# Optimization experiments

Measured on AMD Instinct MI355X. Metric: run time of the kernel, lower is better.

## Reference

```python
import jax, jax.numpy as jnp
import numpy as np

GROUPS = 32
EPS = 1e-5


def setup_inputs() -> dict:
    key = jax.random.key(0)
    ks = jax.random.split(key, 4)
    B, C, H, W = 4, 256, 64, 64
    x = jax.random.normal(ks[0], (B, C, H, W), dtype=jnp.float32)
    gn_w = jnp.ones((C,), jnp.float32)
    gn_b = jnp.zeros((C,), jnp.float32)
    qkv_w = jax.random.normal(ks[1], (3 * C, C), dtype=jnp.float32) * (C ** -0.5)
    qkv_b = jnp.zeros((3 * C,), jnp.float32)
    proj_w = jax.random.normal(ks[2], (C, C), dtype=jnp.float32) * (C ** -0.5)
    proj_b = jnp.zeros((C,), jnp.float32)
    return {"x": x, "gn_w": gn_w, "gn_b": gn_b, "qkv_w": qkv_w,
            "qkv_b": qkv_b, "proj_w": proj_w, "proj_b": proj_b}


def _group_norm(x, w, b):
    B, C, H, W = x.shape
    xr = x.reshape(B, GROUPS, -1)                      # [B, G, (C/G)*H*W]
    mean = xr.mean(axis=-1, keepdims=True)
    var = xr.var(axis=-1, keepdims=True)               # biased, like torch
    h = ((xr - mean) * jax.lax.rsqrt(var + EPS)).reshape(B, C, H, W)
    return h * w[None, :, None, None] + b[None, :, None, None]


def reference(x, gn_w, gn_b, qkv_w, qkv_b, proj_w, proj_b):
    B, C, H, W = x.shape
    h = _group_norm(x, gn_w, gn_b)
    # 1x1 conv == channel GEMM
    qkv = jnp.einsum('oc,bchw->bohw', qkv_w, h) + qkv_b[None, :, None, None]
    qkv = qkv.reshape(B, 3, C, H * W)
    q, k, v = qkv[:, 0], qkv[:, 1], qkv[:, 2]          # [B, C, N]
    scale = C ** (-0.5)
    attn = jax.nn.softmax(jnp.einsum('bci,bcj->bij', q, k) * scale, axis=-1)
    out = jnp.einsum('bij,bcj->bci', attn, v).reshape(B, C, H, W)
    out = jnp.einsum('oc,bchw->bohw', proj_w, out) + proj_b[None, :, None, None]
    return x + out
```

## Files before the change

kernel.cpp:

```cpp
#include <hip/hip_runtime.h>
#include <hip/hip_bf16.h>
#include <math.h>

typedef __bf16 bf16;
typedef __bf16 bf16x8 __attribute__((ext_vector_type(8)));
typedef __bf16 bf16x4 __attribute__((ext_vector_type(4)));
typedef float f32x4 __attribute__((ext_vector_type(4)));
typedef float f32x16 __attribute__((ext_vector_type(16)));

#define MFMA16(a, b, c) __builtin_amdgcn_mfma_f32_16x16x32_bf16(a, b, c, 0, 0, 0)
#define MFMA32(a, b, c) __builtin_amdgcn_mfma_f32_32x32x16_bf16(a, b, c, 0, 0, 0)

#define SCALEK 0.09016844005555896f

typedef const __attribute__((address_space(1))) void* gas_t;
typedef __attribute__((address_space(3))) void* las_t;

__global__ __launch_bounds__(256) void gn_kernel(
    const float* __restrict__ x, const float* __restrict__ gw,
    const float* __restrict__ gb, bf16* __restrict__ h) {
  const int bg = blockIdx.x;
  const int b = bg >> 5, g = bg & 31;
  const size_t base = (size_t)(b * 256 + g * 8) * 4096;
  const float* xp = x + base;
  bf16* hp = h + base;
  const int tid = threadIdx.x;

  float s = 0.f, ss = 0.f;
  for (int i = tid * 4; i < 32768; i += 1024) {
    float4 v = *(const float4*)(xp + i);
    s += v.x + v.y + v.z + v.w;
    ss += v.x * v.x + v.y * v.y + v.z * v.z + v.w * v.w;
  }
#pragma unroll
  for (int off = 32; off; off >>= 1) {
    s += __shfl_down(s, off);
    ss += __shfl_down(ss, off);
  }
  __shared__ float red[8];
  if ((tid & 63) == 0) {
    red[(tid >> 6) * 2] = s;
    red[(tid >> 6) * 2 + 1] = ss;
  }
  __syncthreads();
  s = red[0] + red[2] + red[4] + red[6];
  ss = red[1] + red[3] + red[5] + red[7];
  const float mean = s * (1.f / 32768.f);
  const float var = ss * (1.f / 32768.f) - mean * mean;
  const float rstd = rsqrtf(var + 1e-5f);

  for (int i = tid * 4; i < 32768; i += 1024) {
    float4 v = *(const float4*)(xp + i);
    int c = g * 8 + (i >> 12);
    float a = gw[c] * rstd;
    float b2 = gb[c] - mean * a;
    bf16x4 o;
    o[0] = (bf16)(v.x * a + b2);
    o[1] = (bf16)(v.y * a + b2);
    o[2] = (bf16)(v.z * a + b2);
    o[3] = (bf16)(v.w * a + b2);
    *(bf16x4*)(hp + i) = o;
  }
}

__global__ __launch_bounds__(256) void qkv_gemm(
    const bf16* __restrict__ h, const float* __restrict__ w,
    const float* __restrict__ bias, bf16* __restrict__ qt,
    bf16* __restrict__ kt, bf16* __restrict__ vcm) {
  const int b = blockIdx.z;
  const int o0 = blockIdx.y * 64;
  const int p0 = blockIdx.x * 64;
  __shared__ bf16 Alds[64][56];
  __shared__ bf16 Blds[64][56];
  const int tid = threadIdx.x;
  const int lane = tid & 63, wid = tid >> 6;
  const int lr = lane & 15, lg = lane >> 4;
  const int wm = wid >> 1, wn = wid & 1;
  const bf16* hb = h + (size_t)b * 256 * 4096;

  f32x4 acc[2][2] = {};

  for (int k0 = 0; k0 < 256; k0 += 32) {
    {
      int row = tid >> 2, c8 = (tid & 3) * 8;
      const float* src = w + (size_t)(o0 + row) * 256 + k0 + c8;
      float4 v0 = *(const float4*)src;
      float4 v1 = *(const float4*)(src + 4);
      bf16x8 bv;
      bv[0] = (bf16)v0.x; bv[1] = (bf16)v0.y; bv[2] = (bf16)v0.z; bv[3] = (bf16)v0.w;
      bv[4] = (bf16)v1.x; bv[5] = (bf16)v1.y; bv[6] = (bf16)v1.z; bv[7] = (bf16)v1.w;
      *(bf16x8*)&Alds[row][c8] = bv;
    }
    {
      int cc = tid >> 3, p8 = (tid & 7) * 8;
      bf16x8 v = *(const bf16x8*)(hb + (size_t)(k0 + cc) * 4096 + p0 + p8);
#pragma unroll
      for (int e = 0; e < 8; ++e) Blds[p8 + e][cc] = v[e];
    }
    __syncthreads();
    bf16x8 af[2], bfr[2];
#pragma unroll
    for (int mi = 0; mi < 2; ++mi)
      af[mi] = *(const bf16x8*)&Alds[wm * 32 + mi * 16 + lr][lg * 8];
#pragma unroll
    for (int ni = 0; ni < 2; ++ni)
      bfr[ni] = *(const bf16x8*)&Blds[wn * 32 + ni * 16 + lr][lg * 8];
#pragma unroll
    for (int mi = 0; mi < 2; ++mi)
#pragma unroll
      for (int ni = 0; ni < 2; ++ni)
        acc[mi][ni] = MFMA16(af[mi], bfr[ni], acc[mi][ni]);
    __syncthreads();
  }

#pragma unroll
  for (int mi = 0; mi < 2; ++mi) {
#pragma unroll
    for (int ni = 0; ni < 2; ++ni) {
#pragma unroll
      for (int r = 0; r < 4; ++r) {
        int o = o0 + wm * 32 + mi * 16 + lg * 4 + r;
        int p = p0 + wn * 32 + ni * 16 + lr;
        float val = acc[mi][ni][r] + bias[o];
        if (o < 256) {
          qt[((size_t)b * 4096 + p) * 256 + o] = (bf16)val;
        } else if (o < 512) {
          kt[((size_t)b * 4096 + p) * 256 + (o - 256)] = (bf16)(val * SCALEK);
        } else {
          vcm[((size_t)b * 256 + (o - 512)) * 4096 + p] = (bf16)val;
        }
      }
    }
  }
}

template <int S>
__global__ __launch_bounds__(256, 2) void flash_attn(
    const bf16* __restrict__ qt, const bf16* __restrict__ kt,
    const bf16* __restrict__ vcm, bf16* __restrict__ Opart,
    float* __restrict__ l_g) {
  constexpr int NCOMBO = 4 * S;
  constexpr int CSH = (S == 4) ? 4 : (S == 2) ? 3 : 2;
  constexpr int NIT = (4096 / S) / 32;
  const int bid = blockIdx.x;
  const int combo = bid & (NCOMBO - 1);
  const int qtile = bid >> CSH;
  const int b = combo & 3;
  const int split = combo >> 2;
  const int i0 = qtile * 128;
  const int jbase = split * (4096 / S);

  __shared__ bf16 Klds[2][32][256];
  __shared__ bf16 Vlds[2][256][32];
  const int tid = threadIdx.x;
  const int lane = tid & 63, w = tid >> 6;
  const int ln = lane & 31;
  const int hv = lane >> 5;
  const bf16* qb = qt + (size_t)b * 4096 * 256;
  const bf16* kb = kt + (size_t)b * 4096 * 256;
  const bf16* vb = vcm + (size_t)b * 256 * 4096;

  const int qrow = i0 + w * 32 + ln;
  bf16x8 qf[16];
#pragma unroll
  for (int ks = 0; ks < 16; ++ks)
    qf[ks] = *(const bf16x8*)(qb + (size_t)qrow * 256 + ks * 16 + hv * 8);

  int koff[4], voff[4];
#pragma unroll
  for (int it = 0; it < 4; ++it) {
    int chunk = tid + 256 * it;
    int krow = chunk >> 5;
    koff[it] = krow * 256 + ((((chunk & 31) ^ (krow & 7)) * 8));
    int vrow = chunk >> 2;
    voff[it] = vrow * 4096 + (((chunk & 3) ^ ((vrow >> 2) & 3)) * 8);
  }

#define STAGE_K(JT, BUF)                                                      \
  {                                                                           \
    const int j0s = jbase + (JT) * 32;                                        \
    _Pragma("unroll") for (int it = 0; it < 4; ++it) {                        \
      int chunk = tid + 256 * it;                                             \
      __builtin_amdgcn_global_load_lds(                                       \
          (gas_t)(const void*)(kb + (size_t)j0s * 256 + koff[it]),            \
          (las_t)(void*)(&Klds[BUF][0][0] + chunk * 8), 16, 0, 0);            \
    }                                                                         \
  }
#define STAGE_V(JT, BUF)                                                      \
  {                                                                           \
    const int j0s = jbase + (JT) * 32;                                        \
    _Pragma("unroll") for (int it = 0; it < 4; ++it) {                        \
      int chunk = tid + 256 * it;                                             \
      __builtin_amdgcn_global_load_lds(                                       \
          (gas_t)(const void*)(vb + (size_t)j0s + voff[it]),                  \
          (las_t)(void*)(&Vlds[BUF][0][0] + chunk * 8), 16, 0, 0);            \
    }                                                                         \
  }

  float llane = 0.f;
  f32x16 accO[8] = {};
  const int kswz = ln & 7;
  const int vswz = (ln >> 2) & 3;

  STAGE_K(0, 0);
  STAGE_V(0, 0);
  asm volatile("s_waitcnt vmcnt(0)" ::: "memory");
  __builtin_amdgcn_s_barrier();

  f32x16 a0 = {}, a1 = {};
#pragma unroll
  for (int ks = 0; ks < 8; ++ks) {
    bf16x8 kf0 = *(const bf16x8*)&Klds[0][ln][((2 * ks + hv) ^ kswz) * 8];
    bf16x8 kf1 =
        *(const bf16x8*)&Klds[0][ln][((2 * (ks + 8) + hv) ^ kswz) * 8];
    a0 = MFMA32(kf0, qf[ks], a0);
    a1 = MFMA32(kf1, qf[ks + 8], a1);
  }
  STAGE_K(1, 1);

  for (int t = 0; t < NIT; ++t) {
    asm volatile("s_waitcnt vmcnt(0)" ::: "memory");
    __builtin_amdgcn_s_barrier();

    if (t + 1 < NIT) STAGE_V(t + 1, (t + 1) & 1);
    if (t + 2 < NIT) STAGE_K(t + 2, t & 1);

    float pv[16];
#pragma unroll
    for (int r = 0; r < 16; ++r) pv[r] = exp2f(a0[r] + a1[r]);
    llane += (((pv[0] + pv[1]) + (pv[2] + pv[3])) +
              ((pv[4] + pv[5]) + (pv[6] + pv[7]))) +
             (((pv[8] + pv[9]) + (pv[10] + pv[11])) +
              ((pv[12] + pv[13]) + (pv[14] + pv[15])));

    int pk[8];
#pragma unroll
    for (int q4 = 0; q4 < 8; ++q4)
      asm("v_cvt_pk_bf16_f32 %0, %1, %2"
          : "=v"(pk[q4])
          : "v"(pv[q4 * 2]), "v"(pv[q4 * 2 + 1]));
    bf16x8 pfrag[2];
#pragma unroll
    for (int s = 0; s < 2; ++s) {
      int xa = pk[s * 4 + 0], ya = pk[s * 4 + 2];
      int xb = pk[s * 4 + 1], yb = pk[s * 4 + 3];
      asm("v_permlane32_swap_b32 %0, %1" : "+v"(xa), "+v"(ya));
      asm("v_permlane32_swap_b32 %0, %1" : "+v"(xb), "+v"(yb));
      union { int i[4]; bf16x8 v; } u;
      u.i[0] = xa; u.i[1] = xb; u.i[2] = ya; u.i[3] = yb;
      pfrag[s] = u.v;
    }

    const bf16(*Kc)[256] = Klds[(t + 1) & 1];
    const bf16(*Vc)[32] = Vlds[t & 1];
    __builtin_amdgcn_s_setprio(1);
    if (t + 1 < NIT) {
      f32x16 n0 = {}, n1 = {};
#pragma unroll
      for (int u = 0; u < 8; ++u) {
        bf16x8 kf0 = *(const bf16x8*)&Kc[ln][((2 * u + hv) ^ kswz) * 8];
        n0 = MFMA32(kf0, qf[u], n0);
        bf16x8 kf1 =
            *(const bf16x8*)&Kc[ln][((2 * (u + 8) + hv) ^ kswz) * 8];
        n1 = MFMA32(kf1, qf[u + 8], n1);
        bf16x8 vf0 = *(const bf16x8*)&Vc[u * 32 + ln][((hv) ^ vswz) * 8];
        accO[u] = MFMA32(vf0, pfrag[0], accO[u]);
        bf16x8 vf1 = *(const bf16x8*)&Vc[u * 32 + ln][((2 + hv) ^ vswz) * 8];
        accO[u] = MFMA32(vf1, pfrag[1], accO[u]);
      }
      a0 = n0;
      a1 = n1;
    } else {
#pragma unroll
      for (int u = 0; u < 8; ++u) {
        bf16x8 vf0 = *(const bf16x8*)&Vc[u * 32 + ln][((hv) ^ vswz) * 8];
        accO[u] = MFMA32(vf0, pfrag[0], accO[u]);
        bf16x8 vf1 = *(const bf16x8*)&Vc[u * 32 + ln][((2 + hv) ^ vswz) * 8];
        accO[u] = MFMA32(vf1, pfrag[1], accO[u]);
      }
    }
    __builtin_amdgcn_s_setprio(0);
  }
#undef STAGE_K
#undef STAGE_V

  bf16* ob = Opart + ((size_t)(split * 4 + b) * 4096 + qrow) * 256;
#pragma unroll
  for (int cb = 0; cb < 8; ++cb) {
#pragma unroll
    for (int g = 0; g < 4; ++g) {
      int lo, hi;
      asm("v_cvt_pk_bf16_f32 %0, %1, %2"
          : "=v"(lo)
          : "v"(accO[cb][g * 4 + 0]), "v"(accO[cb][g * 4 + 1]));
      asm("v_cvt_pk_bf16_f32 %0, %1, %2"
          : "=v"(hi)
          : "v"(accO[cb][g * 4 + 2]), "v"(accO[cb][g * 4 + 3]));
      int2 val; val.x = lo; val.y = hi;
      *(int2*)(ob + cb * 32 + g * 8 + hv * 4) = val;
    }
  }
  {
    int xa = __float_as_int(llane);
    int ya = xa;
    asm("v_permlane32_swap_b32 %0, %1" : "+v"(xa), "+v"(ya));
    float ltot = __int_as_float(xa) + __int_as_float(ya);
    if (hv == 0)
      l_g[(size_t)(split * 4 + b) * 4096 + qrow] = ltot;
  }
}

template <int S>
__global__ __launch_bounds__(256) void proj_fused(
    const bf16* __restrict__ Opart, const float* __restrict__ l_g,
    const float* __restrict__ w, const float* __restrict__ bias,
    const float* __restrict__ x, float* __restrict__ out) {
  const int b = blockIdx.z;
  const int o0 = blockIdx.y * 64;
  const int p0 = blockIdx.x * 64;
  __shared__ bf16 Alds[64][56];
  __shared__ bf16 Blds[64][56];
  __shared__ float Linv[64];
  const int tid = threadIdx.x;
  const int lane = tid & 63, wid = tid >> 6;
  const int lr = lane & 15, lg = lane >> 4;
  const int wm = wid >> 1, wn = wid & 1;

  if (tid < 64) {
    float L = 0.f;
#pragma unroll
    for (int s = 0; s < S; ++s)
      L += l_g[(size_t)(s * 4 + b) * 4096 + p0 + tid];
    Linv[tid] = 1.f / L;
  }
  __syncthreads();

  f32x4 acc[2][2] = {};

  for (int k0 = 0; k0 < 256; k0 += 32) {
    {
      int row = tid >> 2, c8 = (tid & 3) * 8;
      const float* src = w + (size_t)(o0 + row) * 256 + k0 + c8;
      float4 v0 = *(const float4*)src;
      float4 v1 = *(const float4*)(src + 4);
      bf16x8 bv;
      bv[0] = (bf16)v0.x; bv[1] = (bf16)v0.y; bv[2] = (bf16)v0.z; bv[3] = (bf16)v0.w;
      bv[4] = (bf16)v1.x; bv[5] = (bf16)v1.y; bv[6] = (bf16)v1.z; bv[7] = (bf16)v1.w;
      *(bf16x8*)&Alds[row][c8] = bv;
    }
    {
      int pr = tid >> 2, c8 = (tid & 3) * 8;
      float a8[8] = {};
#pragma unroll
      for (int s = 0; s < S; ++s) {
        bf16x8 o = *(const bf16x8*)(
            Opart + ((size_t)(s * 4 + b) * 4096 + p0 + pr) * 256 + k0 + c8);
#pragma unroll
        for (int e = 0; e < 8; ++e) a8[e] += (float)o[e];
      }
      float inv = Linv[pr];
      bf16x8 bv;
#pragma unroll
      for (int e = 0; e < 8; ++e) bv[e] = (bf16)(a8[e] * inv);
      *(bf16x8*)&Blds[pr][c8] = bv;
    }
    __syncthreads();
    bf16x8 af[2], bfr[2];
#pragma unroll
    for (int mi = 0; mi < 2; ++mi)
      af[mi] = *(const bf16x8*)&Alds[wm * 32 + mi * 16 + lr][lg * 8];
#pragma unroll
    for (int ni = 0; ni < 2; ++ni)
      bfr[ni] = *(const bf16x8*)&Blds[wn * 32 + ni * 16 + lr][lg * 8];
#pragma unroll
    for (int mi = 0; mi < 2; ++mi)
#pragma unroll
      for (int ni = 0; ni < 2; ++ni)
        acc[mi][ni] = MFMA16(af[mi], bfr[ni], acc[mi][ni]);
    __syncthreads();
  }

#pragma unroll
  for (int mi = 0; mi < 2; ++mi) {
#pragma unroll
    for (int ni = 0; ni < 2; ++ni) {
#pragma unroll
      for (int r = 0; r < 4; ++r) {
        int o = o0 + wm * 32 + mi * 16 + lg * 4 + r;
        int p = p0 + wn * 32 + ni * 16 + lr;
        size_t idx = ((size_t)b * 256 + o) * 4096 + p;
        out[idx] = acc[mi][ni][r] + bias[o] + x[idx];
      }
    }
  }
}

extern "C" void kernel_launch(void* const* d_in, const int* in_sizes, int n_in,
                              void* d_out, int out_size, void* d_ws,
                              size_t ws_size, hipStream_t stream) {
  (void)in_sizes; (void)n_in; (void)out_size;
  const float* x = (const float*)d_in[0];
  const float* gn_w = (const float*)d_in[1];
  const float* gn_b = (const float*)d_in[2];
  const float* qkv_w = (const float*)d_in[3];
  const float* qkv_b = (const float*)d_in[4];
  const float* proj_w = (const float*)d_in[5];
  const float* proj_b = (const float*)d_in[6];
  float* out = (float*)d_out;

  const size_t MB = 1024ull * 1024ull;
  char* ws = (char*)d_ws;
  bf16* h = (bf16*)(ws);
  bf16* qt = (bf16*)(ws + 8 * MB);
  bf16* kt = (bf16*)(ws + 16 * MB);
  bf16* vcm = (bf16*)(ws + 24 * MB);

  int S;
  if (ws_size >= 32 * MB + 4 * 8 * MB + 4ull * 16384 * sizeof(float)) S = 4;
  else if (ws_size >= 32 * MB + 2 * 8 * MB + 2ull * 16384 * sizeof(float)) S = 2;
  else S = 1;

  bf16* Opart = (bf16*)(ws + 32 * MB);
  float* l_g = (float*)(ws + 32 * MB + (size_t)S * 8 * MB);

  gn_kernel<<<128, 256, 0, stream>>>(x, gn_w, gn_b, h);
  qkv_gemm<<<dim3(64, 12, 4), 256, 0, stream>>>(h, qkv_w, qkv_b, qt, kt, vcm);
  if (S == 4) {
    flash_attn<4><<<32 * 16, 256, 0, stream>>>(qt, kt, vcm, Opart, l_g);
    proj_fused<4><<<dim3(64, 4, 4), 256, 0, stream>>>(Opart, l_g, proj_w,
                                                      proj_b, x, out);
  } else if (S == 2) {
    flash_attn<2><<<32 * 8, 256, 0, stream>>>(qt, kt, vcm, Opart, l_g);
    proj_fused<2><<<dim3(64, 4, 4), 256, 0, stream>>>(Opart, l_g, proj_w,
                                                      proj_b, x, out);
  } else {
    flash_attn<1><<<32 * 4, 256, 0, stream>>>(qt, kt, vcm, Opart, l_g);
    proj_fused<1><<<dim3(64, 4, 4), 256, 0, stream>>>(Opart, l_g, proj_w,
                                                      proj_b, x, out);
  }
}
```

Measured before the change: 177.7 us.

## Pre-convert QKV weights, double-buffer QKV GEMM, widen proj tiles to all channels

Adds a kernel that converts the QKV weight matrix to bf16 once per call, so the QKV GEMM can stream A tiles with global_load_lds into a double-buffered LDS, prefetching the next K slice while computing the current one. The projection kernel now has each block cover all 256 output channels for a 64-pixel tile. This makes the split-K partial sums of Opart get read and reduced once instead of four times, and register-prefetches the next K slice. It costs an extra launch, larger per-block LDS and accumulator registers, and fewer proj blocks (256 instead of 1024), which may reduce occupancy.

```diff
diff --git a/kernel.cpp b/kernel.cpp
--- a/kernel.cpp
+++ b/kernel.cpp
@@ -15,6 +15,15 @@
 
 typedef const __attribute__((address_space(1))) void* gas_t;
 typedef __attribute__((address_space(3))) void* las_t;
+
+__global__ __launch_bounds__(256) void wcvt_kernel(const float* __restrict__ qw,
+                                                   bf16* __restrict__ qwb) {
+  int t = blockIdx.x * 256 + threadIdx.x;
+  float4 v = *(const float4*)(qw + (size_t)t * 4);
+  bf16x4 o;
+  o[0] = (bf16)v.x; o[1] = (bf16)v.y; o[2] = (bf16)v.z; o[3] = (bf16)v.w;
+  *(bf16x4*)(qwb + (size_t)t * 4) = o;
+}
 
 __global__ __launch_bounds__(256) void gn_kernel(
     const float* __restrict__ x, const float* __restrict__ gw,
@@ -64,47 +73,54 @@
 }
 
 __global__ __launch_bounds__(256) void qkv_gemm(
-    const bf16* __restrict__ h, const float* __restrict__ w,
+    const bf16* __restrict__ h, const bf16* __restrict__ wb,
     const float* __restrict__ bias, bf16* __restrict__ qt,
     bf16* __restrict__ kt, bf16* __restrict__ vcm) {
   const int b = blockIdx.z;
   const int o0 = blockIdx.y * 64;
   const int p0 = blockIdx.x * 64;
-  __shared__ bf16 Alds[64][56];
-  __shared__ bf16 Blds[64][56];
+  __shared__ bf16 Alds[2][64][32];
+  __shared__ bf16 Blds[2][64][56];
   const int tid = threadIdx.x;
   const int lane = tid & 63, wid = tid >> 6;
   const int lr = lane & 15, lg = lane >> 4;
   const int wm = wid >> 1, wn = wid & 1;
   const bf16* hb = h + (size_t)b * 256 * 4096;
 
+  const int arow = tid >> 2, ac8 = (tid & 3) * 8;
+  const int bcc = tid >> 3, bp8 = (tid & 7) * 8;
+
+#define QKV_STAGE_A(K0, BUF)                                                  \
+  __builtin_amdgcn_global_load_lds(                                           \
+      (gas_t)(const void*)(wb + (size_t)(o0 + arow) * 256 + (K0) + ac8),      \
+      (las_t)(void*)(&Alds[BUF][0][0] + tid * 8), 16, 0, 0);
+
   f32x4 acc[2][2] = {};
 
-  for (int k0 = 0; k0 < 256; k0 += 32) {
-    {
-      int row = tid >> 2, c8 = (tid & 3) * 8;
-      const float* src = w + (size_t)(o0 + row) * 256 + k0 + c8;
-      float4 v0 = *(const float4*)src;
-      float4 v1 = *(const float4*)(src + 4);
-      bf16x8 bv;
-      bv[0] = (bf16)v0.x; bv[1] = (bf16)v0.y; bv[2] = (bf16)v0.z; bv[3] = (bf16)v0.w;
-      bv[4] = (bf16)v1.x; bv[5] = (bf16)v1.y; bv[6] = (bf16)v1.z; bv[7] = (bf16)v1.w;
-      *(bf16x8*)&Alds[row][c8] = bv;
-    }
-    {
-      int cc = tid >> 3, p8 = (tid & 7) * 8;
-      bf16x8 v = *(const bf16x8*)(hb + (size_t)(k0 + cc) * 4096 + p0 + p8);
-#pragma unroll
-      for (int e = 0; e < 8; ++e) Blds[p8 + e][cc] = v[e];
-    }
-    __syncthreads();
+  QKV_STAGE_A(0, 0);
+  {
+    bf16x8 v = *(const bf16x8*)(hb + (size_t)bcc * 4096 + p0 + bp8);
+#pragma unroll
+    for (int e = 0; e < 8; ++e) Blds[0][bp8 + e][bcc] = v[e];
+  }
+  __syncthreads();
+
+  for (int k = 0; k < 8; ++k) {
+    const int cur = k & 1, nb = cur ^ 1;
+    if (k < 7) {
+      QKV_STAGE_A((k + 1) * 32, nb);
+      bf16x8 v =
+          *(const bf16x8*)(hb + (size_t)((k + 1) * 32 + bcc) * 4096 + p0 + bp8);
+#pragma unroll
+      for (int e = 0; e < 8; ++e) Blds[nb][bp8 + e][bcc] = v[e];
+    }
     bf16x8 af[2], bfr[2];
 #pragma unroll
     for (int mi = 0; mi < 2; ++mi)
-      af[mi] = *(const bf16x8*)&Alds[wm * 32 + mi * 16 + lr][lg * 8];
+      af[mi] = *(const bf16x8*)&Alds[cur][wm * 32 + mi * 16 + lr][lg * 8];
 #pragma unroll
     for (int ni = 0; ni < 2; ++ni)
-      bfr[ni] = *(const bf16x8*)&Blds[wn * 32 + ni * 16 + lr][lg * 8];
+      bfr[ni] = *(const bf16x8*)&Blds[cur][wn * 32 + ni * 16 + lr][lg * 8];
 #pragma unroll
     for (int mi = 0; mi < 2; ++mi)
 #pragma unroll
@@ -112,6 +128,7 @@
         acc[mi][ni] = MFMA16(af[mi], bfr[ni], acc[mi][ni]);
     __syncthreads();
   }
+#undef QKV_STAGE_A
 
 #pragma unroll
   for (int mi = 0; mi < 2; ++mi) {
@@ -315,16 +332,14 @@
     const bf16* __restrict__ Opart, const float* __restrict__ l_g,
     const float* __restrict__ w, const float* __restrict__ bias,
     const float* __restrict__ x, float* __restrict__ out) {
-  const int b = blockIdx.z;
-  const int o0 = blockIdx.y * 64;
+  const int b = blockIdx.y;
   const int p0 = blockIdx.x * 64;
-  __shared__ bf16 Alds[64][56];
-  __shared__ bf16 Blds[64][56];
+  __shared__ bf16 Wlds[256][32];
+  __shared__ bf16 Blds[64][32];
   __shared__ float Linv[64];
   const int tid = threadIdx.x;
   const int lane = tid & 63, wid = tid >> 6;
   const int lr = lane & 15, lg = lane >> 4;
-  const int wm = wid >> 1, wn = wid & 1;
 
   if (tid < 64) {
     float L = 0.f;
@@ -335,59 +350,90 @@
   }
   __syncthreads();
 
-  f32x4 acc[2][2] = {};
-
-  for (int k0 = 0; k0 < 256; k0 += 32) {
-    {
-      int row = tid >> 2, c8 = (tid & 3) * 8;
-      const float* src = w + (size_t)(o0 + row) * 256 + k0 + c8;
-      float4 v0 = *(const float4*)src;
-      float4 v1 = *(const float4*)(src + 4);
-      bf16x8 bv;
-      bv[0] = (bf16)v0.x; bv[1] = (bf16)v0.y; bv[2] = (bf16)v0.z; bv[3] = (bf16)v0.w;
-      bv[4] = (bf16)v1.x; bv[5] = (bf16)v1.y; bv[6] = (bf16)v1.z; bv[7] = (bf16)v1.w;
-      *(bf16x8*)&Alds[row][c8] = bv;
-    }
-    {
-      int pr = tid >> 2, c8 = (tid & 3) * 8;
-      float a8[8] = {};
-#pragma unroll
-      for (int s = 0; s < S; ++s) {
-        bf16x8 o = *(const bf16x8*)(
-            Opart + ((size_t)(s * 4 + b) * 4096 + p0 + pr) * 256 + k0 + c8);
-#pragma unroll
-        for (int e = 0; e < 8; ++e) a8[e] += (float)o[e];
-      }
-      float inv = Linv[pr];
-      bf16x8 bv;
-#pragma unroll
-      for (int e = 0; e < 8; ++e) bv[e] = (bf16)(a8[e] * inv);
-      *(bf16x8*)&Blds[pr][c8] = bv;
-    }
+  const int pr = tid >> 2, c8b = (tid & 3) * 8;
+  const float invp = Linv[pr];
+
+  float4 wreg[4][2];
+  bf16x8 breg[S];
+
+#define PROJ_READ(K0)                                                         \
+  {                                                                           \
+    _Pragma("unroll") for (int it = 0; it < 4; ++it) {                        \
+      int chunk = tid + 256 * it;                                             \
+      int row = chunk >> 2, c8 = (chunk & 3) * 8;                             \
+      const float* src = w + (size_t)row * 256 + (K0) + c8;                   \
+      wreg[it][0] = *(const float4*)src;                                      \
+      wreg[it][1] = *(const float4*)(src + 4);                                \
+    }                                                                         \
+    _Pragma("unroll") for (int s = 0; s < S; ++s) breg[s] =                   \
+        *(const bf16x8*)(Opart +                                              \
+                         ((size_t)(s * 4 + b) * 4096 + p0 + pr) * 256 +       \
+                         (K0) + c8b);                                         \
+  }
+#define PROJ_WRITE()                                                          \
+  {                                                                           \
+    _Pragma("unroll") for (int it = 0; it < 4; ++it) {                        \
+      int chunk = tid + 256 * it;                                             \
+      int row = chunk >> 2, c8 = (chunk & 3) * 8;                             \
+      bf16x8 bv;                                                              \
+      bv[0] = (bf16)wreg[it][0].x; bv[1] = (bf16)wreg[it][0].y;               \
+      bv[2] = (bf16)wreg[it][0].z; bv[3] = (bf16)wreg[it][0].w;               \
+      bv[4] = (bf16)wreg[it][1].x; bv[5] = (bf16)wreg[it][1].y;               \
+      bv[6] = (bf16)wreg[it][1].z; bv[7] = (bf16)wreg[it][1].w;               \
+      *(bf16x8*)&Wlds[row][c8] = bv;                                          \
+    }                                                                         \
+    {                                                                         \
+      float a8[8] = {};                                                       \
+      _Pragma("unroll") for (int s = 0; s < S; ++s) {                         \
+        _Pragma("unroll") for (int e = 0; e < 8; ++e) a8[e] +=                \
+            (float)breg[s][e];                                                \
+      }                                                                       \
+      bf16x8 bv;                                                              \
+      _Pragma("unroll") for (int e = 0; e < 8; ++e) bv[e] =                   \
+          (bf16)(a8[e] * invp);                                               \
+      *(bf16x8*)&Blds[pr][c8b] = bv;                                          \
+    }                                                                         \
+  }
+
+  f32x4 acc[4][4] = {};
+
+  PROJ_READ(0);
+  PROJ_WRITE();
+  __syncthreads();
+
+  for (int k = 0; k < 8; ++k) {
+    if (k < 7) PROJ_READ((k + 1) * 32);
+
+    bf16x8 af[4], bfr[4];
+#pragma unroll
+    for (int mi = 0; mi < 4; ++mi)
+      af[mi] = *(const bf16x8*)&Wlds[wid * 64 + mi * 16 + lr][lg * 8];
+#pragma unroll
+    for (int ni = 0; ni < 4; ++ni)
+      bfr[ni] = *(const bf16x8*)&Blds[ni * 16 + lr][lg * 8];
+#pragma unroll
+    for (int mi = 0; mi < 4; ++mi)
+#pragma unroll
+      for (int ni = 0; ni < 4; ++ni)
+        acc[mi][ni] = MFMA16(af[mi], bfr[ni], acc[mi][ni]);
+
     __syncthreads();
-    bf16x8 af[2], bfr[2];
-#pragma unroll
-    for (int mi = 0; mi < 2; ++mi)
-      af[mi] = *(const bf16x8*)&Alds[wm * 32 + mi * 16 + lr][lg * 8];
-#pragma unroll
-    for (int ni = 0; ni < 2; ++ni)
-      bfr[ni] = *(const bf16x8*)&Blds[wn * 32 + ni * 16 + lr][lg * 8];
-#pragma unroll
-    for (int mi = 0; mi < 2; ++mi)
-#pragma unroll
-      for (int ni = 0; ni < 2; ++ni)
-        acc[mi][ni] = MFMA16(af[mi], bfr[ni], acc[mi][ni]);
-    __syncthreads();
-  }
-
-#pragma unroll
-  for (int mi = 0; mi < 2; ++mi) {
-#pragma unroll
-    for (int ni = 0; ni < 2; ++ni) {
+    if (k < 7) {
+      PROJ_WRITE();
+      __syncthreads();
+    }
+  }
+#undef PROJ_READ
+#undef PROJ_WRITE
+
+#pragma unroll
+  for (int mi = 0; mi < 4; ++mi) {
+#pragma unroll
+    for (int ni = 0; ni < 4; ++ni) {
 #pragma unroll
       for (int r = 0; r < 4; ++r) {
-        int o = o0 + wm * 32 + mi * 16 + lg * 4 + r;
-        int p = p0 + wn * 32 + ni * 16 + lr;
+        int o = wid * 64 + mi * 16 + lg * 4 + r;
+        int p = p0 + ni * 16 + lr;
         size_t idx = ((size_t)b * 256 + o) * 4096 + p;
         out[idx] = acc[mi][ni][r] + bias[o] + x[idx];
       }
@@ -420,22 +466,33 @@
   else if (ws_size >= 32 * MB + 2 * 8 * MB + 2ull * 16384 * sizeof(float)) S = 2;
   else S = 1;
 
-  bf16* Opart = (bf16*)(ws + 32 * MB);
-  float* l_g = (float*)(ws + 32 * MB + (size_t)S * 8 * MB);
-
+  bf16* Opart;
+  float* l_g;
+  bf16* qwb;
+  if (S >= 2) {
+    Opart = (bf16*)(ws + 32 * MB);
+    l_g = (float*)(ws + 32 * MB + (size_t)S * 8 * MB);
+    qwb = Opart;
+  } else {
+    Opart = h;
+    l_g = (float*)(ws + 32 * MB);
+    qwb = (bf16*)(ws + 32 * MB + 256 * 1024);
+  }
+
+  wcvt_kernel<<<192, 256, 0, stream>>>(qkv_w, qwb);
   gn_kernel<<<128, 256, 0, stream>>>(x, gn_w, gn_b, h);
-  qkv_gemm<<<dim3(64, 12, 4), 256, 0, stream>>>(h, qkv_w, qkv_b, qt, kt, vcm);
+  qkv_gemm<<<dim3(64, 12, 4), 256, 0, stream>>>(h, qwb, qkv_b, qt, kt, vcm);
   if (S == 4) {
     flash_attn<4><<<32 * 16, 256, 0, stream>>>(qt, kt, vcm, Opart, l_g);
-    proj_fused<4><<<dim3(64, 4, 4), 256, 0, stream>>>(Opart, l_g, proj_w,
-                                                      proj_b, x, out);
+    proj_fused<4><<<dim3(64, 4), 256, 0, stream>>>(Opart, l_g, proj_w, proj_b,
+                                                   x, out);
   } else if (S == 2) {
     flash_attn<2><<<32 * 8, 256, 0, stream>>>(qt, kt, vcm, Opart, l_g);
-    proj_fused<2><<<dim3(64, 4, 4), 256, 0, stream>>>(Opart, l_g, proj_w,
-                                                      proj_b, x, out);
+    proj_fused<2><<<dim3(64, 4), 256, 0, stream>>>(Opart, l_g, proj_w, proj_b,
+                                                   x, out);
   } else {
     flash_attn<1><<<32 * 4, 256, 0, stream>>>(qt, kt, vcm, Opart, l_g);
-    proj_fused<1><<<dim3(64, 4, 4), 256, 0, stream>>>(Opart, l_g, proj_w,
-                                                      proj_b, x, out);
-  }
-}
+    proj_fused<1><<<dim3(64, 4), 256, 0, stream>>>(Opart, l_g, proj_w, proj_b,
+                                                   x, out);
+  }
+}
```

Result: no change. 180.1 us (+1.4%).
